# Kernel optimization log

Measured on AMD Instinct MI355X. Metric: run time of the kernel, lower is better.

## Reference

```python
import jax, jax.numpy as jnp
import numpy as np
from jax import lax

WINDOW_SIZE = 11
SIGMA = 1.5
VAL_RANGE = 1000.0 / 10.0  # L = 100.0


def _gaussian_window(window_size, sigma, channel):
    # matches torch: exp(-(x - ws//2)^2 / (2*sigma^2)), normalized
    x = np.arange(window_size, dtype=np.float32)
    g = np.exp(-((x - window_size // 2) ** 2) / (2.0 * sigma ** 2))
    g = g / g.sum()
    w2d = np.outer(g, g).astype(np.float32)  # [ws, ws]
    # depthwise kernel, OIHW with I=1, O=channel
    w = np.broadcast_to(w2d, (channel, 1, window_size, window_size))
    return jnp.asarray(np.ascontiguousarray(w))


def _depthwise_conv(x, window, channel):
    # x: [B, C, H, W], window: [C, 1, ws, ws], valid padding, groups=C
    return lax.conv_general_dilated(
        x, window,
        window_strides=(1, 1), padding='VALID',
        dimension_numbers=('NCHW', 'OIHW', 'NCHW'),
        feature_group_count=channel)


def setup_inputs() -> dict:
    key = jax.random.key(0)
    k1, k2 = jax.random.split(key)
    B, C, H, W = 32, 1, 480, 640
    img1 = jax.random.uniform(k1, (B, C, H, W), dtype=jnp.float32)
    img2 = jax.random.uniform(k2, (B, C, H, W), dtype=jnp.float32)
    return {"img1": img1, "img2": img2}


def reference(img1, img2):
    channel = img1.shape[1]
    window = _gaussian_window(WINDOW_SIZE, SIGMA, channel)

    L = VAL_RANGE
    C1 = (0.01 * L) ** 2
    C2 = (0.03 * L) ** 2

    mu1 = _depthwise_conv(img1, window, channel)
    mu2 = _depthwise_conv(img2, window, channel)
    mu1_sq = mu1 * mu1
    mu2_sq = mu2 * mu2
    mu1_mu2 = mu1 * mu2

    sigma1_sq = _depthwise_conv(img1 * img1, window, channel) - mu1_sq
    sigma2_sq = _depthwise_conv(img2 * img2, window, channel) - mu2_sq
    sigma12 = _depthwise_conv(img1 * img2, window, channel) - mu1_mu2

    v1 = 2.0 * sigma12 + C2
    v2 = sigma1_sq + sigma2_sq + C2
    ssim_map = (2.0 * mu1_mu2 + C1) * v1 / ((mu1_sq + mu2_sq + C1) * v2)

    ret = jnp.mean(ssim_map)  # size_average=True
    L_ssim = (1.0 - ret) / 2.0
    return L_ssim
```

## Files before the change

kernel.cpp:

```cpp
#include <hip/hip_runtime.h>

#define IMG_H 480
#define IMG_W 640
#define OUT_H 470
#define OUT_W 630
#define NBATCH 32
#define SW 54
#define NSTRIPE 12
#define RCH 30
#define NCHUNK 16
#define NROWS (RCH + 10)

#define SSIM_C1 1.0f
#define SSIM_C2 9.0f

__device__ constexpr float WG[11] = {
    0.00102838f, 0.00759876f, 0.03600077f, 0.10936068f, 0.21300554f,
    0.26601173f,
    0.21300554f, 0.10936068f, 0.03600077f, 0.00759876f, 0.00102838f
};

__device__ __forceinline__ float lane_shift(int baddr, int j, float v) {
    return __int_as_float(
        __builtin_amdgcn_ds_bpermute(baddr + (j << 2), __float_as_int(v)));
}

#define PHASE(P, IT)                                                          \
  {                                                                           \
    const int it = (IT);                                                      \
             \
    float n1 = 0.f, n2 = 0.f;                                                 \
    if (it + 1 < NROWS) {                                                     \
      int gy = y0 + it + 1; if (gy > IMG_H - 1) gy = IMG_H - 1;               \
      const float* __restrict__ r1 = p1 + gy * IMG_W;                         \
      const float* __restrict__ r2 = p2 + gy * IMG_W;                         \
      n1 = r1[colA]; n2 = r2[colA];                                           \
    }                                                                         \
      \
    float h1 = 0.f, h2 = 0.f, h11 = 0.f, h22 = 0.f, h12 = 0.f;                \
    _Pragma("unroll")                                                         \
    for (int j = 0; j < 11; ++j) {                                            \
      float v1 = (j == 0) ? c1 : lane_shift(baddr, j, c1);                    \
      float v2 = (j == 0) ? c2 : lane_shift(baddr, j, c2);                    \
      float t1 = WG[j] * v1, t2 = WG[j] * v2;                                 \
      h1 += t1; h2 += t2;                                                     \
      h11 = fmaf(t1, v1, h11);                                                \
      h22 = fmaf(t2, v2, h22);                                                \
      h12 = fmaf(t1, v2, h12);                                                \
    }                                                                         \
            \
    _Pragma("unroll")                                                         \
    for (int sl = 0; sl < 11; ++sl) {                                         \
      const float wt = WG[((P) - sl + 11) % 11];                              \
      acc[sl][0] = fmaf(wt, h1,  acc[sl][0]);                                 \
      acc[sl][1] = fmaf(wt, h2,  acc[sl][1]);                                 \
      acc[sl][2] = fmaf(wt, h11, acc[sl][2]);                                 \
      acc[sl][3] = fmaf(wt, h22, acc[sl][3]);                                 \
      acc[sl][4] = fmaf(wt, h12, acc[sl][4]);                                 \
    }                                                                         \
           \
    const int sc = ((P) + 1) % 11;                                            \
    const int y = it - 10;                                                    \
    if (it >= 10 && (y0 + y) < OUT_H && valid_col) {                          \
      float m1 = acc[sc][0], m2 = acc[sc][1];                                 \
      float mu1s = m1 * m1, mu2s = m2 * m2, mu12 = m1 * m2;                   \
      float vA = 2.f * (acc[sc][4] - mu12) + SSIM_C2;                         \
      float vB = (acc[sc][2] - mu1s) + (acc[sc][3] - mu2s) + SSIM_C2;         \
      float num = (2.f * mu12 + SSIM_C1) * vA;                                \
      float den = (mu1s + mu2s + SSIM_C1) * vB;                               \
      lsum = fmaf(num, __builtin_amdgcn_rcpf(den), lsum);                     \
    }                                                                         \
    acc[sc][0] = 0.f; acc[sc][1] = 0.f; acc[sc][2] = 0.f;                     \
    acc[sc][3] = 0.f; acc[sc][4] = 0.f;                                       \
    c1 = n1; c2 = n2;                                                         \
  }

__global__ __launch_bounds__(64, 4) void ssim_main(
    const float* __restrict__ img1,
    const float* __restrict__ img2,
    float* __restrict__ partials)
{
    const int lane   = threadIdx.x;
    const int stripe = blockIdx.x;
    const int cy     = blockIdx.y;
    const int b      = blockIdx.z;
    const int x0 = SW * stripe;
    const int y0 = RCH * cy;

    const float* __restrict__ p1 = img1 + (size_t)b * (IMG_H * IMG_W);
    const float* __restrict__ p2 = img2 + (size_t)b * (IMG_H * IMG_W);

    int colA = x0 + lane;  if (colA > IMG_W - 1) colA = IMG_W - 1;
    const int baddr = lane << 2;

    const bool valid_col = (lane < SW) && (x0 + lane < OUT_W);

    float acc[11][5];
#pragma unroll
    for (int i = 0; i < 11; ++i)
#pragma unroll
        for (int j = 0; j < 5; ++j) acc[i][j] = 0.f;

    float lsum = 0.f;

    float c1, c2;
    {
        const float* __restrict__ r1 = p1 + y0 * IMG_W;
        const float* __restrict__ r2 = p2 + y0 * IMG_W;
        c1 = r1[colA]; c2 = r2[colA];
    }

    for (int blk = 0; blk < 3; ++blk) {
        const int base = blk * 11;
#pragma unroll
        for (int p = 0; p < 11; ++p) PHASE(p, base + p)
    }
    {
        const int base = 33;
#pragma unroll
        for (int p = 0; p < 7; ++p) PHASE(p, base + p)
    }

#pragma unroll
    for (int off = 32; off > 0; off >>= 1)
        lsum += __shfl_down(lsum, off);
    if (lane == 0)
        partials[(b * NCHUNK + cy) * NSTRIPE + stripe] = lsum;
}

__global__ __launch_bounds__(256) void ssim_reduce(
    const float* __restrict__ partials, float* __restrict__ out)
{
    const int n = NSTRIPE * NCHUNK * NBATCH;
    __shared__ double red[256];
    int tid = threadIdx.x;
    double s = 0.0;
    for (int i = tid; i < n; i += 256) s += (double)partials[i];
    red[tid] = s;
    __syncthreads();
    for (int k = 128; k > 0; k >>= 1) {
        if (tid < k) red[tid] += red[tid + k];
        __syncthreads();
    }
    if (tid == 0) {
        double mean = red[0] / (double)((size_t)NBATCH * OUT_H * OUT_W);
        out[0] = (float)((1.0 - mean) * 0.5);
    }
}

extern "C" void kernel_launch(void* const* d_in, const int* in_sizes, int n_in,
                              void* d_out, int out_size, void* d_ws, size_t ws_size,
                              hipStream_t stream)
{
    const float* img1 = (const float*)d_in[0];
    const float* img2 = (const float*)d_in[1];
    float* out = (float*)d_out;
    float* partials = (float*)d_ws;

    dim3 grid(NSTRIPE, NCHUNK, NBATCH);
    ssim_main<<<grid, dim3(64), 0, stream>>>(img1, img2, partials);
    ssim_reduce<<<1, dim3(256), 0, stream>>>(partials, out);
}
```

Measured before the change: 151.4 us.

## Process two adjacent columns per lane with float2 loads to widen stripes

```diff
diff --git a/kernel.cpp b/kernel.cpp
--- a/kernel.cpp
+++ b/kernel.cpp
@@ -5,8 +5,8 @@
 #define OUT_H 470
 #define OUT_W 630
 #define NBATCH 32
-#define SW 54
-#define NSTRIPE 12
+#define SW 118
+#define NSTRIPE 6
 #define RCH 30
 #define NCHUNK 16
 #define NROWS (RCH + 10)
@@ -28,54 +28,74 @@
 #define PHASE(P, IT)                                                          \
   {                                                                           \
     const int it = (IT);                                                      \
-             \
-    float n1 = 0.f, n2 = 0.f;                                                 \
+         \
+    float2 n1 = make_float2(0.f, 0.f), n2 = n1;                               \
     if (it + 1 < NROWS) {                                                     \
       int gy = y0 + it + 1; if (gy > IMG_H - 1) gy = IMG_H - 1;               \
-      const float* __restrict__ r1 = p1 + gy * IMG_W;                         \
-      const float* __restrict__ r2 = p2 + gy * IMG_W;                         \
-      n1 = r1[colA]; n2 = r2[colA];                                           \
+      n1 = *(const float2*)(p1 + gy * IMG_W + colA);                          \
+      n2 = *(const float2*)(p2 + gy * IMG_W + colA);                          \
     }                                                                         \
-      \
-    float h1 = 0.f, h2 = 0.f, h11 = 0.f, h22 = 0.f, h12 = 0.f;                \
+           \
+    float v1[12], v2[12];                                                     \
+    v1[0] = c1.x; v1[1] = c1.y; v2[0] = c2.x; v2[1] = c2.y;                   \
+    _Pragma("unroll")                                                         \
+    for (int j = 1; j <= 5; ++j) {                                            \
+      v1[2*j]   = lane_shift(baddr, j, c1.x);                                 \
+      v1[2*j+1] = lane_shift(baddr, j, c1.y);                                 \
+      v2[2*j]   = lane_shift(baddr, j, c2.x);                                 \
+      v2[2*j+1] = lane_shift(baddr, j, c2.y);                                 \
+    }                                                                         \
+     \
+    float h1A=0.f,h2A=0.f,h11A=0.f,h22A=0.f,h12A=0.f;                         \
+    float h1B=0.f,h2B=0.f,h11B=0.f,h22B=0.f,h12B=0.f;                         \
     _Pragma("unroll")                                                         \
     for (int j = 0; j < 11; ++j) {                                            \
-      float v1 = (j == 0) ? c1 : lane_shift(baddr, j, c1);                    \
-      float v2 = (j == 0) ? c2 : lane_shift(baddr, j, c2);                    \
-      float t1 = WG[j] * v1, t2 = WG[j] * v2;                                 \
-      h1 += t1; h2 += t2;                                                     \
-      h11 = fmaf(t1, v1, h11);                                                \
-      h22 = fmaf(t2, v2, h22);                                                \
-      h12 = fmaf(t1, v2, h12);                                                \
+      float a1 = v1[j], a2 = v2[j];                                           \
+      float t1 = WG[j] * a1, t2 = WG[j] * a2;                                 \
+      h1A += t1; h2A += t2;                                                   \
+      h11A = fmaf(t1, a1, h11A);                                              \
+      h22A = fmaf(t2, a2, h22A);                                              \
+      h12A = fmaf(t1, a2, h12A);                                              \
+      float b1 = v1[j+1], b2 = v2[j+1];                                       \
+      float u1 = WG[j] * b1, u2 = WG[j] * b2;                                 \
+      h1B += u1; h2B += u2;                                                   \
+      h11B = fmaf(u1, b1, h11B);                                              \
+      h22B = fmaf(u2, b2, h22B);                                              \
+      h12B = fmaf(u1, b2, h12B);                                              \
     }                                                                         \
             \
     _Pragma("unroll")                                                         \
     for (int sl = 0; sl < 11; ++sl) {                                         \
       const float wt = WG[((P) - sl + 11) % 11];                              \
-      acc[sl][0] = fmaf(wt, h1,  acc[sl][0]);                                 \
-      acc[sl][1] = fmaf(wt, h2,  acc[sl][1]);                                 \
-      acc[sl][2] = fmaf(wt, h11, acc[sl][2]);                                 \
-      acc[sl][3] = fmaf(wt, h22, acc[sl][3]);                                 \
-      acc[sl][4] = fmaf(wt, h12, acc[sl][4]);                                 \
+      acc[sl][0][0]=fmaf(wt,h1A, acc[sl][0][0]); acc[sl][0][1]=fmaf(wt,h1B, acc[sl][0][1]); \
+      acc[sl][1][0]=fmaf(wt,h2A, acc[sl][1][0]); acc[sl][1][1]=fmaf(wt,h2B, acc[sl][1][1]); \
+      acc[sl][2][0]=fmaf(wt,h11A,acc[sl][2][0]); acc[sl][2][1]=fmaf(wt,h11B,acc[sl][2][1]); \
+      acc[sl][3][0]=fmaf(wt,h22A,acc[sl][3][0]); acc[sl][3][1]=fmaf(wt,h22B,acc[sl][3][1]); \
+      acc[sl][4][0]=fmaf(wt,h12A,acc[sl][4][0]); acc[sl][4][1]=fmaf(wt,h12B,acc[sl][4][1]); \
     }                                                                         \
            \
     const int sc = ((P) + 1) % 11;                                            \
     const int y = it - 10;                                                    \
-    if (it >= 10 && (y0 + y) < OUT_H && valid_col) {                          \
-      float m1 = acc[sc][0], m2 = acc[sc][1];                                 \
-      float mu1s = m1 * m1, mu2s = m2 * m2, mu12 = m1 * m2;                   \
-      float vA = 2.f * (acc[sc][4] - mu12) + SSIM_C2;                         \
-      float vB = (acc[sc][2] - mu1s) + (acc[sc][3] - mu2s) + SSIM_C2;         \
-      float num = (2.f * mu12 + SSIM_C1) * vA;                                \
-      float den = (mu1s + mu2s + SSIM_C1) * vB;                               \
-      lsum = fmaf(num, __builtin_amdgcn_rcpf(den), lsum);                     \
+    if (it >= 10 && (y0 + y) < OUT_H) {                                       \
+      _Pragma("unroll")                                                       \
+      for (int s = 0; s < 2; ++s) {                                           \
+        if (s == 0 ? validA : validB) {                                       \
+          float m1 = acc[sc][0][s], m2 = acc[sc][1][s];                       \
+          float mu1s = m1 * m1, mu2s = m2 * m2, mu12 = m1 * m2;               \
+          float vA = 2.f * (acc[sc][4][s] - mu12) + SSIM_C2;                  \
+          float vB = (acc[sc][2][s] - mu1s) + (acc[sc][3][s] - mu2s) + SSIM_C2; \
+          float num = (2.f * mu12 + SSIM_C1) * vA;                            \
+          float den = (mu1s + mu2s + SSIM_C1) * vB;                           \
+          lsum = fmaf(num, __builtin_amdgcn_rcpf(den), lsum);                 \
+        }                                                                     \
+      }                                                                       \
     }                                                                         \
-    acc[sc][0] = 0.f; acc[sc][1] = 0.f; acc[sc][2] = 0.f;                     \
-    acc[sc][3] = 0.f; acc[sc][4] = 0.f;                                       \
+    _Pragma("unroll")                                                         \
+    for (int ch = 0; ch < 5; ++ch) { acc[sc][ch][0] = 0.f; acc[sc][ch][1] = 0.f; } \
     c1 = n1; c2 = n2;                                                         \
   }
 
-__global__ __launch_bounds__(64, 4) void ssim_main(
+__global__ __launch_bounds__(64, 3) void ssim_main(
     const float* __restrict__ img1,
     const float* __restrict__ img2,
     float* __restrict__ partials)
@@ -90,24 +110,24 @@
     const float* __restrict__ p1 = img1 + (size_t)b * (IMG_H * IMG_W);
     const float* __restrict__ p2 = img2 + (size_t)b * (IMG_H * IMG_W);
 
-    int colA = x0 + lane;  if (colA > IMG_W - 1) colA = IMG_W - 1;
+    int colA = x0 + 2 * lane;  if (colA > IMG_W - 2) colA = IMG_W - 2;
     const int baddr = lane << 2;
 
-    const bool valid_col = (lane < SW) && (x0 + lane < OUT_W);
+    const bool validA = (lane < 59) && (x0 + 2 * lane     < OUT_W);
+    const bool validB = (lane < 59) && (x0 + 2 * lane + 1 < OUT_W);
 
-    float acc[11][5];
+    float acc[11][5][2];
 #pragma unroll
     for (int i = 0; i < 11; ++i)
 #pragma unroll
-        for (int j = 0; j < 5; ++j) acc[i][j] = 0.f;
+        for (int j = 0; j < 5; ++j) { acc[i][j][0] = 0.f; acc[i][j][1] = 0.f; }
 
     float lsum = 0.f;
 
-    float c1, c2;
+    float2 c1, c2;
     {
-        const float* __restrict__ r1 = p1 + y0 * IMG_W;
-        const float* __restrict__ r2 = p2 + y0 * IMG_W;
-        c1 = r1[colA]; c2 = r2[colA];
+        c1 = *(const float2*)(p1 + y0 * IMG_W + colA);
+        c2 = *(const float2*)(p2 + y0 * IMG_W + colA);
     }
 
     for (int blk = 0; blk < 3; ++blk) {
```

Result: slower. 189.1 us (+24.8%).
